# Kernel optimization log

Hardware: AMD Instinct MI355X
Metric: run time of the kernel (lower is better)

The kernel has to match this reference:

```python
import jax, jax.numpy as jnp
import numpy as np

H, B, T, DH = 16, 2, 2048, 64
MODEL_DIM = 1024


def setup_inputs() -> dict:
    key = jax.random.key(0)
    ks = jax.random.split(key, 5)
    q = jax.random.normal(ks[0], (H, B, T, DH), dtype=jnp.float32)
    k = jax.random.normal(ks[1], (H, B, T, DH), dtype=jnp.float32)
    v = jax.random.normal(ks[2], (H, B, T, DH), dtype=jnp.float32)
    Wo_w = jax.random.normal(ks[3], (MODEL_DIM, H * DH), dtype=jnp.float32) * 0.02
    Wo_b = jax.random.normal(ks[4], (MODEL_DIM,), dtype=jnp.float32) * 0.02
    return {"q": q, "k": k, "v": v, "Wo_w": Wo_w, "Wo_b": Wo_b}


def reference(q, k, v, Wo_w, Wo_b):
    # per-head scaled dot-product attention; scale uses per-head dk (=DH)
    scale = jnp.sqrt(jnp.asarray(DH, dtype=q.dtype))
    # scores: [H, B, T, T]
    scores = jnp.einsum('hbtd,hbsd->hbts', q, k) / scale
    # causal mask (additive -1e12 on strict upper triangle, matching torch code)
    mask = jnp.triu(jnp.ones((T, T), dtype=bool), 1)
    scores = scores + (-1e12) * mask.astype(scores.dtype)
    weights = jax.nn.softmax(scores, axis=-1)
    # context per head: [H, B, T, DH]
    context = jnp.einsum('hbts,hbsd->hbtd', weights, v)
    # concat heads along feature dim: [B, T, H*DH]
    context = jnp.transpose(context, (1, 2, 0, 3)).reshape(B, T, H * DH)
    # output projection (torch Linear: x @ W.T + b)
    return context @ Wo_w.T + Wo_b
```

## Files before the change

### kernel.cpp

```cpp
#include <hip/hip_runtime.h>

typedef __attribute__((ext_vector_type(8))) short bf16x8;
typedef __attribute__((ext_vector_type(4))) float f32x4;
typedef __attribute__((ext_vector_type(4))) unsigned int u32x4;
typedef __attribute__((ext_vector_type(2))) unsigned int u32x2;
typedef __attribute__((ext_vector_type(4))) unsigned short u16x4;

#define H_ 16
#define B_ 2
#define T_ 2048
#define DH_ 64
#define MD_ 1024

static __device__ inline unsigned short f2bf(float f) {
    union { float f; unsigned u; } x; x.f = f;
    unsigned r = (x.u + 0x7fffu + ((x.u >> 16) & 1u)) >> 16;
    return (unsigned short)r;
}
static __device__ inline unsigned int pack_bf2(float lo, float hi) {
    return __builtin_amdgcn_perm(__float_as_uint(hi), __float_as_uint(lo), 0x07060302u);
}
static __device__ inline float fexp2(float x) {
#if __has_builtin(__builtin_amdgcn_exp2f)
    return __builtin_amdgcn_exp2f(x);
#else
    return exp2f(x);
#endif
}

__global__ __launch_bounds__(256) void prep_k(const float* __restrict__ k,
                                              const float* __restrict__ v,
                                              const float* __restrict__ w,
                                              unsigned short* __restrict__ kb,
                                              unsigned short* __restrict__ vtb,
                                              unsigned short* __restrict__ wob,
                                              int* __restrict__ fl) {
    __shared__ __attribute__((aligned(16))) unsigned short vt64[64][64];
    const int blk = blockIdx.x;
    const int tid = threadIdx.x;
    if (blk < 1024) {
        int i = (blk * 256 + tid) * 4;
        f32x4 x = *(const f32x4*)(w + i);
        u16x4 y;
        y[0] = f2bf(x[0]); y[1] = f2bf(x[1]); y[2] = f2bf(x[2]); y[3] = f2bf(x[3]);
        *(u16x4*)(wob + i) = y;
    } else if (blk < 2048) {
        int j = blk - 1024;
        const int hb = j >> 5, s0 = (j & 31) * 64;
        const int row = tid >> 2, c = (tid & 3) * 16;
        const long off = (long)hb * (T_ * DH_) + (long)(s0 + row) * DH_ + c;
        const float* p = k + off;
        f32x4 a0 = *(const f32x4*)p;
        f32x4 a1 = *(const f32x4*)(p + 4);
        f32x4 a2 = *(const f32x4*)(p + 8);
        f32x4 a3 = *(const f32x4*)(p + 12);
        u32x4 w0, w1;
        w0[0] = pack_bf2(a0[0], a0[1]); w0[1] = pack_bf2(a0[2], a0[3]);
        w0[2] = pack_bf2(a1[0], a1[1]); w0[3] = pack_bf2(a1[2], a1[3]);
        w1[0] = pack_bf2(a2[0], a2[1]); w1[1] = pack_bf2(a2[2], a2[3]);
        w1[2] = pack_bf2(a3[0], a3[1]); w1[3] = pack_bf2(a3[2], a3[3]);
        *(u32x4*)(kb + off) = w0;
        *(u32x4*)(kb + off + 8) = w1;
    } else if (blk < 3072) {
        int j = blk - 2048;
        const int hb = j >> 5, s0 = (j & 31) * 64;
        const int vkp = tid & 31, vdg = tid >> 5;
        const float* vp = v + (long)hb * (T_ * DH_) + (long)(s0 + 2 * vkp) * DH_ + vdg * 8;
        f32x4 va0 = *(const f32x4*)vp;
        f32x4 va1 = *(const f32x4*)(vp + 4);
        f32x4 vb0 = *(const f32x4*)(vp + DH_);
        f32x4 vb1 = *(const f32x4*)(vp + DH_ + 4);
#pragma unroll
        for (int jj = 0; jj < 4; jj++) {
            ((unsigned int*)&vt64[vdg * 8 + jj][0])[vkp]     = pack_bf2(va0[jj], vb0[jj]);
            ((unsigned int*)&vt64[vdg * 8 + 4 + jj][0])[vkp] = pack_bf2(va1[jj], vb1[jj]);
        }
        __syncthreads();
        const int dh = tid >> 2, kc = (tid & 3) * 16;
        u32x4 o0 = *(const u32x4*)&vt64[dh][kc];
        u32x4 o1 = *(const u32x4*)&vt64[dh][kc + 8];
        unsigned short* op = vtb + (long)hb * (DH_ * T_) + (long)dh * T_ + s0 + kc;
        *(u32x4*)op = o0;
        *(u32x4*)(op + 8) = o1;
    } else {
        for (int z = tid; z < 256; z += 256) fl[z] = 0;
    }
}

#define SE2(t, lo, hi) ((unsigned)((t) | ((lo) << 4) | ((hi) << 10)))
__constant__ unsigned sched24[3][8] = {
    { SE2(15,0,16), SE2(7,0,16), SE2(14,0,15), SE2(14,15,30),
      SE2(13,0,14), SE2(13,14,28), SE2(12,13,26), SE2(11,12,24) },
    { SE2(15,16,32), SE2(6,0,14), SE2(12,0,13), SE2(10,0,11),
      SE2(10,11,22), SE2(9,0,10), SE2(11,0,12), SE2(5,0,12) },
    { SE2(0,0,2), SE2(1,0,4), SE2(2,0,6), SE2(3,0,8),
      SE2(8,0,9), SE2(9,10,20), SE2(8,9,18), SE2(4,0,10) },
};

__global__ __launch_bounds__(256, 3) void attn_k(const float* __restrict__ q,
                                                 const unsigned short* __restrict__ kb,
                                                 const unsigned short* __restrict__ vtb,
                                                 unsigned short* __restrict__ ctx,
                                                 float* __restrict__ Op,
                                                 float* __restrict__ lp,
                                                 int* __restrict__ fl) {
    const int i = blockIdx.x;
    const int xcd = i & 7, j = i >> 3;
    const int cu = j & 31, slot = j >> 5;
    const int type = cu >> 2, hbl = cu & 3;
    const unsigned e = sched24[slot][type];
    const int t  = (int)(e & 15u);
    const int lo = (int)((e >> 4) & 63u);
    const int hi = (int)(e >> 10);
    const int hb = xcd * 4 + hbl;
    const int h = hb >> 1, b = hb & 1;
    const int tid = threadIdx.x;
    const int wave = tid >> 6, lane = tid & 63;
    const int ln = lane & 15, quad = lane >> 4;

    __shared__ __attribute__((aligned(16))) unsigned short kt[64][72];
    __shared__ __attribute__((aligned(16))) unsigned short vt[64][72];
    __shared__ __attribute__((aligned(16))) unsigned short pl[4][32][72];
    __shared__ int sh_who;

    const long kbase = (long)hb * (T_ * DH_);
    const long vbase = (long)hb * (DH_ * T_);
    const int q0w = t * 128 + wave * 32;
    const int srow = tid >> 2, sc = (tid & 3) * 16;

    bf16x8 qf00, qf01, qf10, qf11;
    {
        const float qs = 0.18033688011112042f;
        const float* qp0 = q + kbase + (long)(q0w + ln) * DH_ + quad * 8;
        const float* qp1 = qp0 + 16 * DH_;
        f32x4 a0 = *(const f32x4*)qp0;
        f32x4 a1 = *(const f32x4*)(qp0 + 4);
        f32x4 b0 = *(const f32x4*)(qp0 + 32);
        f32x4 b1 = *(const f32x4*)(qp0 + 36);
        f32x4 c0 = *(const f32x4*)qp1;
        f32x4 c1 = *(const f32x4*)(qp1 + 4);
        f32x4 d0 = *(const f32x4*)(qp1 + 32);
        f32x4 d1 = *(const f32x4*)(qp1 + 36);
#pragma unroll
        for (int z = 0; z < 4; z++) {
            qf00[z]   = (short)f2bf(a0[z] * qs);
            qf00[4+z] = (short)f2bf(a1[z] * qs);
            qf01[z]   = (short)f2bf(b0[z] * qs);
            qf01[4+z] = (short)f2bf(b1[z] * qs);
            qf10[z]   = (short)f2bf(c0[z] * qs);
            qf10[4+z] = (short)f2bf(c1[z] * qs);
            qf11[z]   = (short)f2bf(d0[z] * qs);
            qf11[4+z] = (short)f2bf(d1[z] * qs);
        }
    }

    f32x4 oT0[4], oT1[4];
#pragma unroll
    for (int z = 0; z < 4; z++) { oT0[z] = f32x4{0.f,0.f,0.f,0.f}; oT1[z] = f32x4{0.f,0.f,0.f,0.f}; }
    float lsum0 = 0.f, lsum1 = 0.f;

    u32x4 kr0, kr1, vr0, vr1;
    {
        const unsigned short* kp = kb + kbase + (long)(lo * 64 + srow) * DH_ + sc;
        kr0 = *(const u32x4*)kp; kr1 = *(const u32x4*)(kp + 8);
        const unsigned short* vp = vtb + vbase + (long)srow * T_ + lo * 64 + sc;
        vr0 = *(const u32x4*)vp; vr1 = *(const u32x4*)(vp + 8);
    }

#pragma unroll 1
    for (int step = lo; step < hi; step++) {
        __syncthreads();
        *(u32x4*)&kt[srow][sc]     = kr0;
        *(u32x4*)&kt[srow][sc + 8] = kr1;
        *(u32x4*)&vt[srow][sc]     = vr0;
        *(u32x4*)&vt[srow][sc + 8] = vr1;
        __syncthreads();

        if (step + 1 < hi) {
            const unsigned short* kp = kb + kbase + (long)((step + 1) * 64 + srow) * DH_ + sc;
            kr0 = *(const u32x4*)kp; kr1 = *(const u32x4*)(kp + 8);
            const unsigned short* vp = vtb + vbase + (long)srow * T_ + (step + 1) * 64 + sc;
            vr0 = *(const u32x4*)vp; vr1 = *(const u32x4*)(vp + 8);
        }

        if (step * 64 <= q0w + 31) {
            const bool dmask = (step * 64 + 63 > q0w);
            const int dbase = step * 64 + quad * 4 - q0w - ln;

#pragma unroll
            for (int nt = 0; nt < 4; nt++) {
                bf16x8 kf0 = *(const bf16x8*)&kt[nt * 16 + ln][quad * 8];
                bf16x8 kf1 = *(const bf16x8*)&kt[nt * 16 + ln][32 + quad * 8];
                f32x4 a0 = f32x4{0.f,0.f,0.f,0.f};
                a0 = __builtin_amdgcn_mfma_f32_16x16x32_bf16(kf0, qf00, a0, 0, 0, 0);
                a0 = __builtin_amdgcn_mfma_f32_16x16x32_bf16(kf1, qf01, a0, 0, 0, 0);
                f32x4 a1 = f32x4{0.f,0.f,0.f,0.f};
                a1 = __builtin_amdgcn_mfma_f32_16x16x32_bf16(kf0, qf10, a1, 0, 0, 0);
                a1 = __builtin_amdgcn_mfma_f32_16x16x32_bf16(kf1, qf11, a1, 0, 0, 0);
#pragma unroll
                for (int r = 0; r < 4; r++) { a0[r] = fexp2(a0[r]); a1[r] = fexp2(a1[r]); }
                if (dmask) {
#pragma unroll
                    for (int r = 0; r < 4; r++) {
                        if (dbase + nt * 16 + r > 0)  a0[r] = 0.f;
                        if (dbase + nt * 16 + r > 16) a1[r] = 0.f;
                    }
                }
                lsum0 += (a0[0] + a0[1]) + (a0[2] + a0[3]);
                lsum1 += (a1[0] + a1[1]) + (a1[2] + a1[3]);
                u32x2 w0, w1;
                w0[0] = pack_bf2(a0[0], a0[1]); w0[1] = pack_bf2(a0[2], a0[3]);
                w1[0] = pack_bf2(a1[0], a1[1]); w1[1] = pack_bf2(a1[2], a1[3]);
                *(u32x2*)&pl[wave][ln][nt * 16 + quad * 4]      = w0;
                *(u32x2*)&pl[wave][16 + ln][nt * 16 + quad * 4] = w1;
            }

            bf16x8 pf00 = *(const bf16x8*)&pl[wave][ln][quad * 8];
            bf16x8 pf01 = *(const bf16x8*)&pl[wave][ln][32 + quad * 8];
            bf16x8 pf10 = *(const bf16x8*)&pl[wave][16 + ln][quad * 8];
            bf16x8 pf11 = *(const bf16x8*)&pl[wave][16 + ln][32 + quad * 8];

#pragma unroll
            for (int dt = 0; dt < 4; dt++) {
                bf16x8 vf0 = *(const bf16x8*)&vt[dt * 16 + ln][quad * 8];
                bf16x8 vf1 = *(const bf16x8*)&vt[dt * 16 + ln][32 + quad * 8];
                oT0[dt] = __builtin_amdgcn_mfma_f32_16x16x32_bf16(vf0, pf00, oT0[dt], 0, 0, 0);
                oT0[dt] = __builtin_amdgcn_mfma_f32_16x16x32_bf16(vf1, pf01, oT0[dt], 0, 0, 0);
                oT1[dt] = __builtin_amdgcn_mfma_f32_16x16x32_bf16(vf0, pf10, oT1[dt], 0, 0, 0);
                oT1[dt] = __builtin_amdgcn_mfma_f32_16x16x32_bf16(vf1, pf11, oT1[dt], 0, 0, 0);
            }
        }
    }

    lsum0 += __shfl_xor(lsum0, 16); lsum0 += __shfl_xor(lsum0, 32);
    lsum1 += __shfl_xor(lsum1, 16); lsum1 += __shfl_xor(lsum1, 32);

    float rl0, rl1;
    if (t < 8) {
        rl0 = __builtin_amdgcn_rcpf(lsum0);
        rl1 = __builtin_amdgcn_rcpf(lsum1);
    } else {
        const int c = (lo != 0) ? 1 : 0;
        const long slab = ((long)c * 32 + hb) * 8 + (t - 8);
        float* ob = Op + slab * 8192;
        const int ql0 = wave * 32 + ln, ql1 = ql0 + 16;
#pragma unroll
        for (int dt = 0; dt < 4; dt++)
#pragma unroll
            for (int r = 0; r < 4; r++) {
                const int dh = dt * 16 + quad * 4 + r;
                __hip_atomic_store(&ob[dh * 128 + ql0], oT0[dt][r],
                                   __ATOMIC_RELAXED, __HIP_MEMORY_SCOPE_AGENT);
                __hip_atomic_store(&ob[dh * 128 + ql1], oT1[dt][r],
                                   __ATOMIC_RELAXED, __HIP_MEMORY_SCOPE_AGENT);
            }
        if (quad == 0) {
            __hip_atomic_store(&lp[slab * 128 + ql0], lsum0,
                               __ATOMIC_RELAXED, __HIP_MEMORY_SCOPE_AGENT);
            __hip_atomic_store(&lp[slab * 128 + ql1], lsum1,
                               __ATOMIC_RELAXED, __HIP_MEMORY_SCOPE_AGENT);
        }
        __syncthreads();
        if (tid == 0)
            sh_who = __hip_atomic_fetch_add(&fl[hb * 8 + (t - 8)], 1,
                                            __ATOMIC_RELAXED, __HIP_MEMORY_SCOPE_AGENT);
        __syncthreads();
        if (sh_who != 1) return;
        const long slab2 = ((long)(c ^ 1) * 32 + hb) * 8 + (t - 8);
        const float* qb = Op + slab2 * 8192;
#pragma unroll
        for (int dt = 0; dt < 4; dt++)
#pragma unroll
            for (int r = 0; r < 4; r++) {
                const int dh = dt * 16 + quad * 4 + r;
                oT0[dt][r] += __hip_atomic_load(&qb[dh * 128 + ql0],
                                                __ATOMIC_RELAXED, __HIP_MEMORY_SCOPE_AGENT);
                oT1[dt][r] += __hip_atomic_load(&qb[dh * 128 + ql1],
                                                __ATOMIC_RELAXED, __HIP_MEMORY_SCOPE_AGENT);
            }
        lsum0 += __hip_atomic_load(&lp[slab2 * 128 + ql0],
                                   __ATOMIC_RELAXED, __HIP_MEMORY_SCOPE_AGENT);
        lsum1 += __hip_atomic_load(&lp[slab2 * 128 + ql1],
                                   __ATOMIC_RELAXED, __HIP_MEMORY_SCOPE_AGENT);
        rl0 = __builtin_amdgcn_rcpf(lsum0);
        rl1 = __builtin_amdgcn_rcpf(lsum1);
    }

#pragma unroll
    for (int dt = 0; dt < 4; dt++) {
        u16x4 y0, y1;
        y0[0] = f2bf(oT0[dt][0] * rl0); y0[1] = f2bf(oT0[dt][1] * rl0);
        y0[2] = f2bf(oT0[dt][2] * rl0); y0[3] = f2bf(oT0[dt][3] * rl0);
        y1[0] = f2bf(oT1[dt][0] * rl1); y1[1] = f2bf(oT1[dt][1] * rl1);
        y1[2] = f2bf(oT1[dt][2] * rl1); y1[3] = f2bf(oT1[dt][3] * rl1);
        *(u16x4*)&pl[wave][ln][dt * 16 + quad * 4]      = y0;
        *(u16x4*)&pl[wave][16 + ln][dt * 16 + quad * 4] = y1;
    }
    const int rr = lane >> 1, cc = (lane & 1) * 32;
    u32x4 z0 = *(const u32x4*)&pl[wave][rr][cc];
    u32x4 z1 = *(const u32x4*)&pl[wave][rr][cc + 8];
    u32x4 z2 = *(const u32x4*)&pl[wave][rr][cc + 16];
    u32x4 z3 = *(const u32x4*)&pl[wave][rr][cc + 24];
    unsigned short* cp = ctx + (long)(b * T_ + t * 128 + wave * 32 + rr) * MD_ + h * 64 + cc;
    *(u32x4*)cp = z0;
    *(u32x4*)(cp + 8) = z1;
    *(u32x4*)(cp + 16) = z2;
    *(u32x4*)(cp + 24) = z3;
}

__global__ __launch_bounds__(256, 4) void proj_k(const unsigned short* __restrict__ A,
                                                 const unsigned short* __restrict__ Bw,
                                                 const float* __restrict__ bias,
                                                 float* __restrict__ out) {
    const int i = blockIdx.x;
    const int n0 = ((i & 7) * 2 + ((i >> 3) & 1)) * 64;
    const int m0 = (i >> 4) * 64;
    const int tid = threadIdx.x;
    const int wave = tid >> 6, lane = tid & 63;
    const int ln = lane & 15, quad = lane >> 4;

    __shared__ __attribute__((aligned(16))) unsigned short As[64][72];
    __shared__ __attribute__((aligned(16))) unsigned short Bs[64][72];

    const int srow = tid >> 2, sc = (tid & 3) * 16;

    f32x4 acc[4];
#pragma unroll
    for (int z = 0; z < 4; z++) acc[z] = f32x4{0.f, 0.f, 0.f, 0.f};

    u32x4 ar0, ar1, br0, br1;
    {
        const unsigned short* ap = A + (long)(m0 + srow) * 1024 + sc;
        ar0 = *(const u32x4*)ap; ar1 = *(const u32x4*)(ap + 8);
        const unsigned short* bp = Bw + (long)(n0 + srow) * 1024 + sc;
        br0 = *(const u32x4*)bp; br1 = *(const u32x4*)(bp + 8);
    }

#pragma unroll 1
    for (int ks = 0; ks < 1024; ks += 64) {
        __syncthreads();
        *(u32x4*)&As[srow][sc]     = ar0;
        *(u32x4*)&As[srow][sc + 8] = ar1;
        *(u32x4*)&Bs[srow][sc]     = br0;
        *(u32x4*)&Bs[srow][sc + 8] = br1;
        __syncthreads();

        if (ks + 64 < 1024) {
            const unsigned short* ap = A + (long)(m0 + srow) * 1024 + ks + 64 + sc;
            ar0 = *(const u32x4*)ap; ar1 = *(const u32x4*)(ap + 8);
            const unsigned short* bp = Bw + (long)(n0 + srow) * 1024 + ks + 64 + sc;
            br0 = *(const u32x4*)bp; br1 = *(const u32x4*)(bp + 8);
        }

        bf16x8 bf0 = *(const bf16x8*)&Bs[wave * 16 + ln][quad * 8];
        bf16x8 bf1 = *(const bf16x8*)&Bs[wave * 16 + ln][32 + quad * 8];
#pragma unroll
        for (int mt = 0; mt < 4; mt++) {
            bf16x8 af0 = *(const bf16x8*)&As[mt * 16 + ln][quad * 8];
            bf16x8 af1 = *(const bf16x8*)&As[mt * 16 + ln][32 + quad * 8];
            acc[mt] = __builtin_amdgcn_mfma_f32_16x16x32_bf16(af0, bf0, acc[mt], 0, 0, 0);
            acc[mt] = __builtin_amdgcn_mfma_f32_16x16x32_bf16(af1, bf1, acc[mt], 0, 0, 0);
        }
    }

    int col = n0 + wave * 16 + ln;
    float bz = bias[col];
#pragma unroll
    for (int mt = 0; mt < 4; mt++)
#pragma unroll
        for (int r = 0; r < 4; r++) {
            int row = m0 + mt * 16 + quad * 4 + r;
            out[(long)row * 1024 + col] = acc[mt][r] + bz;
        }
}

extern "C" void kernel_launch(void* const* d_in, const int* in_sizes, int n_in,
                              void* d_out, int out_size, void* d_ws, size_t ws_size,
                              hipStream_t stream) {
    const float* q    = (const float*)d_in[0];
    const float* k    = (const float*)d_in[1];
    const float* v    = (const float*)d_in[2];
    const float* Wo_w = (const float*)d_in[3];
    const float* Wo_b = (const float*)d_in[4];
    float* out = (float*)d_out;

    unsigned short* ctx = (unsigned short*)d_ws;
    unsigned short* wob = ctx + (size_t)4096 * 1024;
    unsigned short* kbb = wob + (size_t)1024 * 1024;
    unsigned short* vtb = kbb + (size_t)32 * 2048 * 64;
    float* Opart = (float*)(vtb + (size_t)32 * 2048 * 64);
    float* lpart = Opart + (size_t)2 * 32 * 8 * 64 * 128;
    int*   flags = (int*)(lpart + (size_t)2 * 32 * 8 * 128);

    prep_k<<<3073, 256, 0, stream>>>(k, v, Wo_w, kbb, vtb, wob, flags);
    attn_k<<<768, 256, 0, stream>>>(q, kbb, vtb, ctx, Opart, lpart, flags);
    proj_k<<<1024, 256, 0, stream>>>(ctx, wob, Wo_b, out);
}
```

Measured before the change: 150.5 us.

## Replace static block-to-chunk schedule with per-XCD atomic work queue ordered longest-first

Instead of mapping each block to a fixed (slot,type) entry from a static 3x8 schedule, each block takes a ticket from a per-XCD atomic counter. It then picks work chunks from a list sorted by decreasing cost, so long causal query tiles start first and short ones fill the tail. The counters sit in the flag buffer, which the prep kernel now zeroes over a longer range. This adds one global atomic and a block barrier per block, and it relies on dispatch order for good balance.

```diff
diff --git a/kernel.cpp b/kernel.cpp
--- a/kernel.cpp
+++ b/kernel.cpp
@@ -83,18 +83,21 @@
         *(u32x4*)op = o0;
         *(u32x4*)(op + 8) = o1;
     } else {
-        for (int z = tid; z < 256; z += 256) fl[z] = 0;
+        for (int z = tid; z < 264; z += 256) fl[z] = 0;
     }
 }
 
 #define SE2(t, lo, hi) ((unsigned)((t) | ((lo) << 4) | ((hi) << 10)))
-__constant__ unsigned sched24[3][8] = {
-    { SE2(15,0,16), SE2(7,0,16), SE2(14,0,15), SE2(14,15,30),
-      SE2(13,0,14), SE2(13,14,28), SE2(12,13,26), SE2(11,12,24) },
-    { SE2(15,16,32), SE2(6,0,14), SE2(12,0,13), SE2(10,0,11),
-      SE2(10,11,22), SE2(9,0,10), SE2(11,0,12), SE2(5,0,12) },
-    { SE2(0,0,2), SE2(1,0,4), SE2(2,0,6), SE2(3,0,8),
-      SE2(8,0,9), SE2(9,10,20), SE2(8,9,18), SE2(4,0,10) },
+__constant__ unsigned chunk24[24] = {
+    SE2(15,0,16), SE2(15,16,32), SE2(7,0,16),
+    SE2(14,0,15), SE2(14,15,30),
+    SE2(13,0,14), SE2(13,14,28), SE2(6,0,14),
+    SE2(12,0,13), SE2(12,13,26),
+    SE2(11,0,12), SE2(11,12,24), SE2(5,0,12),
+    SE2(10,0,11), SE2(10,11,22),
+    SE2(9,0,10),  SE2(9,10,20),  SE2(4,0,10),
+    SE2(8,0,9),   SE2(8,9,18),
+    SE2(3,0,8), SE2(2,0,6), SE2(1,0,4), SE2(0,0,2)
 };
 
 __global__ __launch_bounds__(256, 3) void attn_k(const float* __restrict__ q,
@@ -104,24 +107,29 @@
                                                  float* __restrict__ Op,
                                                  float* __restrict__ lp,
                                                  int* __restrict__ fl) {
-    const int i = blockIdx.x;
-    const int xcd = i & 7, j = i >> 3;
-    const int cu = j & 31, slot = j >> 5;
-    const int type = cu >> 2, hbl = cu & 3;
-    const unsigned e = sched24[slot][type];
+    const int xcd = blockIdx.x & 7;
+    const int tid = threadIdx.x;
+
+    __shared__ __attribute__((aligned(16))) unsigned short kt[64][72];
+    __shared__ __attribute__((aligned(16))) unsigned short vt[64][72];
+    __shared__ __attribute__((aligned(16))) unsigned short pl[4][32][72];
+    __shared__ int sh_who;
+    __shared__ int sh_slot;
+
+    if (tid == 0)
+        sh_slot = __hip_atomic_fetch_add(&fl[256 + xcd], 1,
+                                         __ATOMIC_RELAXED, __HIP_MEMORY_SCOPE_AGENT);
+    __syncthreads();
+    const int slot = sh_slot;
+    const unsigned e = chunk24[slot >> 2];
+    const int hbl = slot & 3;
     const int t  = (int)(e & 15u);
     const int lo = (int)((e >> 4) & 63u);
     const int hi = (int)(e >> 10);
     const int hb = xcd * 4 + hbl;
     const int h = hb >> 1, b = hb & 1;
-    const int tid = threadIdx.x;
     const int wave = tid >> 6, lane = tid & 63;
     const int ln = lane & 15, quad = lane >> 4;
-
-    __shared__ __attribute__((aligned(16))) unsigned short kt[64][72];
-    __shared__ __attribute__((aligned(16))) unsigned short vt[64][72];
-    __shared__ __attribute__((aligned(16))) unsigned short pl[4][32][72];
-    __shared__ int sh_who;
 
     const long kbase = (long)hb * (T_ * DH_);
     const long vbase = (long)hb * (DH_ * T_);
```

Result: slower. 160.6 us (+6.7%).

## Load K/V fragments directly from global per wave, drop shared staging

Applied to the files above, without the earlier changes.

Removes the block-wide shared-memory staging of K and V tiles, along with its two barriers per step and the register prefetch. Each wave now loads its own MFMA fragments straight from global memory and runs only up to its own causal bound, so waves skip tiles that lie fully above the diagonal. This removes synchronisation and the LDS round trip, but each wave loads the K/V tile separately, raising global/L2 traffic, and the next tile is no longer prefetched, which exposes load latency.

```diff
diff --git a/kernel.cpp b/kernel.cpp
--- a/kernel.cpp
+++ b/kernel.cpp
@@ -118,15 +118,12 @@
     const int wave = tid >> 6, lane = tid & 63;
     const int ln = lane & 15, quad = lane >> 4;
 
-    __shared__ __attribute__((aligned(16))) unsigned short kt[64][72];
-    __shared__ __attribute__((aligned(16))) unsigned short vt[64][72];
     __shared__ __attribute__((aligned(16))) unsigned short pl[4][32][72];
     __shared__ int sh_who;
 
     const long kbase = (long)hb * (T_ * DH_);
     const long vbase = (long)hb * (DH_ * T_);
     const int q0w = t * 128 + wave * 32;
-    const int srow = tid >> 2, sc = (tid & 3) * 16;
 
     bf16x8 qf00, qf01, qf10, qf11;
     {
@@ -159,76 +156,65 @@
     for (int z = 0; z < 4; z++) { oT0[z] = f32x4{0.f,0.f,0.f,0.f}; oT1[z] = f32x4{0.f,0.f,0.f,0.f}; }
     float lsum0 = 0.f, lsum1 = 0.f;
 
-    u32x4 kr0, kr1, vr0, vr1;
-    {
-        const unsigned short* kp = kb + kbase + (long)(lo * 64 + srow) * DH_ + sc;
-        kr0 = *(const u32x4*)kp; kr1 = *(const u32x4*)(kp + 8);
-        const unsigned short* vp = vtb + vbase + (long)srow * T_ + lo * 64 + sc;
-        vr0 = *(const u32x4*)vp; vr1 = *(const u32x4*)(vp + 8);
-    }
+    const int hiw = min(hi, 2 * t + 1 + (wave >> 1));
 
 #pragma unroll 1
-    for (int step = lo; step < hi; step++) {
-        __syncthreads();
-        *(u32x4*)&kt[srow][sc]     = kr0;
-        *(u32x4*)&kt[srow][sc + 8] = kr1;
-        *(u32x4*)&vt[srow][sc]     = vr0;
-        *(u32x4*)&vt[srow][sc + 8] = vr1;
-        __syncthreads();
-
-        if (step + 1 < hi) {
-            const unsigned short* kp = kb + kbase + (long)((step + 1) * 64 + srow) * DH_ + sc;
-            kr0 = *(const u32x4*)kp; kr1 = *(const u32x4*)(kp + 8);
-            const unsigned short* vp = vtb + vbase + (long)srow * T_ + (step + 1) * 64 + sc;
-            vr0 = *(const u32x4*)vp; vr1 = *(const u32x4*)(vp + 8);
-        }
-
-        if (step * 64 <= q0w + 31) {
-            const bool dmask = (step * 64 + 63 > q0w);
-            const int dbase = step * 64 + quad * 4 - q0w - ln;
-
-#pragma unroll
-            for (int nt = 0; nt < 4; nt++) {
-                bf16x8 kf0 = *(const bf16x8*)&kt[nt * 16 + ln][quad * 8];
-                bf16x8 kf1 = *(const bf16x8*)&kt[nt * 16 + ln][32 + quad * 8];
-                f32x4 a0 = f32x4{0.f,0.f,0.f,0.f};
-                a0 = __builtin_amdgcn_mfma_f32_16x16x32_bf16(kf0, qf00, a0, 0, 0, 0);
-                a0 = __builtin_amdgcn_mfma_f32_16x16x32_bf16(kf1, qf01, a0, 0, 0, 0);
-                f32x4 a1 = f32x4{0.f,0.f,0.f,0.f};
-                a1 = __builtin_amdgcn_mfma_f32_16x16x32_bf16(kf0, qf10, a1, 0, 0, 0);
-                a1 = __builtin_amdgcn_mfma_f32_16x16x32_bf16(kf1, qf11, a1, 0, 0, 0);
-#pragma unroll
-                for (int r = 0; r < 4; r++) { a0[r] = fexp2(a0[r]); a1[r] = fexp2(a1[r]); }
-                if (dmask) {
-#pragma unroll
-                    for (int r = 0; r < 4; r++) {
-                        if (dbase + nt * 16 + r > 0)  a0[r] = 0.f;
-                        if (dbase + nt * 16 + r > 16) a1[r] = 0.f;
-                    }
+    for (int step = lo; step < hiw; step++) {
+        const unsigned short* kp0 = kb + kbase + (long)(step * 64 + ln) * DH_ + quad * 8;
+        bf16x8 kfr[8];
+#pragma unroll
+        for (int nt = 0; nt < 4; nt++) {
+            kfr[2*nt]     = *(const bf16x8*)(kp0 + nt * 16 * DH_);
+            kfr[2*nt + 1] = *(const bf16x8*)(kp0 + nt * 16 * DH_ + 32);
+        }
+        const unsigned short* vp0 = vtb + vbase + (long)ln * T_ + step * 64 + quad * 8;
+        bf16x8 vfr[8];
+#pragma unroll
+        for (int dt = 0; dt < 4; dt++) {
+            vfr[2*dt]     = *(const bf16x8*)(vp0 + dt * 16 * T_);
+            vfr[2*dt + 1] = *(const bf16x8*)(vp0 + dt * 16 * T_ + 32);
+        }
+
+        const bool dmask = (step * 64 + 63 > q0w);
+        const int dbase = step * 64 + quad * 4 - q0w - ln;
+
+#pragma unroll
+        for (int nt = 0; nt < 4; nt++) {
+            f32x4 a0 = f32x4{0.f,0.f,0.f,0.f};
+            a0 = __builtin_amdgcn_mfma_f32_16x16x32_bf16(kfr[2*nt], qf00, a0, 0, 0, 0);
+            a0 = __builtin_amdgcn_mfma_f32_16x16x32_bf16(kfr[2*nt+1], qf01, a0, 0, 0, 0);
+            f32x4 a1 = f32x4{0.f,0.f,0.f,0.f};
+            a1 = __builtin_amdgcn_mfma_f32_16x16x32_bf16(kfr[2*nt], qf10, a1, 0, 0, 0);
+            a1 = __builtin_amdgcn_mfma_f32_16x16x32_bf16(kfr[2*nt+1], qf11, a1, 0, 0, 0);
+#pragma unroll
+            for (int r = 0; r < 4; r++) { a0[r] = fexp2(a0[r]); a1[r] = fexp2(a1[r]); }
+            if (dmask) {
+#pragma unroll
+                for (int r = 0; r < 4; r++) {
+                    if (dbase + nt * 16 + r > 0)  a0[r] = 0.f;
+                    if (dbase + nt * 16 + r > 16) a1[r] = 0.f;
                 }
-                lsum0 += (a0[0] + a0[1]) + (a0[2] + a0[3]);
-                lsum1 += (a1[0] + a1[1]) + (a1[2] + a1[3]);
-                u32x2 w0, w1;
-                w0[0] = pack_bf2(a0[0], a0[1]); w0[1] = pack_bf2(a0[2], a0[3]);
-                w1[0] = pack_bf2(a1[0], a1[1]); w1[1] = pack_bf2(a1[2], a1[3]);
-                *(u32x2*)&pl[wave][ln][nt * 16 + quad * 4]      = w0;
-                *(u32x2*)&pl[wave][16 + ln][nt * 16 + quad * 4] = w1;
             }
-
-            bf16x8 pf00 = *(const bf16x8*)&pl[wave][ln][quad * 8];
-            bf16x8 pf01 = *(const bf16x8*)&pl[wave][ln][32 + quad * 8];
-            bf16x8 pf10 = *(const bf16x8*)&pl[wave][16 + ln][quad * 8];
-            bf16x8 pf11 = *(const bf16x8*)&pl[wave][16 + ln][32 + quad * 8];
-
-#pragma unroll
-            for (int dt = 0; dt < 4; dt++) {
-                bf16x8 vf0 = *(const bf16x8*)&vt[dt * 16 + ln][quad * 8];
-                bf16x8 vf1 = *(const bf16x8*)&vt[dt * 16 + ln][32 + quad * 8];
-                oT0[dt] = __builtin_amdgcn_mfma_f32_16x16x32_bf16(vf0, pf00, oT0[dt], 0, 0, 0);
-                oT0[dt] = __builtin_amdgcn_mfma_f32_16x16x32_bf16(vf1, pf01, oT0[dt], 0, 0, 0);
-                oT1[dt] = __builtin_amdgcn_mfma_f32_16x16x32_bf16(vf0, pf10, oT1[dt], 0, 0, 0);
-                oT1[dt] = __builtin_amdgcn_mfma_f32_16x16x32_bf16(vf1, pf11, oT1[dt], 0, 0, 0);
-            }
+            lsum0 += (a0[0] + a0[1]) + (a0[2] + a0[3]);
+            lsum1 += (a1[0] + a1[1]) + (a1[2] + a1[3]);
+            u32x2 w0, w1;
+            w0[0] = pack_bf2(a0[0], a0[1]); w0[1] = pack_bf2(a0[2], a0[3]);
+            w1[0] = pack_bf2(a1[0], a1[1]); w1[1] = pack_bf2(a1[2], a1[3]);
+            *(u32x2*)&pl[wave][ln][nt * 16 + quad * 4]      = w0;
+            *(u32x2*)&pl[wave][16 + ln][nt * 16 + quad * 4] = w1;
+        }
+
+        bf16x8 pf00 = *(const bf16x8*)&pl[wave][ln][quad * 8];
+        bf16x8 pf01 = *(const bf16x8*)&pl[wave][ln][32 + quad * 8];
+        bf16x8 pf10 = *(const bf16x8*)&pl[wave][16 + ln][quad * 8];
+        bf16x8 pf11 = *(const bf16x8*)&pl[wave][16 + ln][32 + quad * 8];
+
+#pragma unroll
+        for (int dt = 0; dt < 4; dt++) {
+            oT0[dt] = __builtin_amdgcn_mfma_f32_16x16x32_bf16(vfr[2*dt], pf00, oT0[dt], 0, 0, 0);
+            oT0[dt] = __builtin_amdgcn_mfma_f32_16x16x32_bf16(vfr[2*dt+1], pf01, oT0[dt], 0, 0, 0);
+            oT1[dt] = __builtin_amdgcn_mfma_f32_16x16x32_bf16(vfr[2*dt], pf10, oT1[dt], 0, 0, 0);
+            oT1[dt] = __builtin_amdgcn_mfma_f32_16x16x32_bf16(vfr[2*dt+1], pf11, oT1[dt], 0, 0, 0);
         }
     }
 
```

New measurement: 186.5 us. 23.9% more time.
